# Performance work log

Measured on AMD Instinct MI355X. Metric: run time of the kernel, lower is better.

## Reference

```python
import jax, jax.numpy as jnp
import numpy as np
from jax import lax

N = 8192          # river-network nodes
B = 2             # batch
T = 1024          # time steps (hours)
W = 64            # max_delay (IRF support)
H = 256           # MLP hidden dim
DT = 1.0 / 24.0   # dt in days
D_LEVELS = 8      # tree depth (4-ary tree with 8192 nodes -> depths 0..7)
BRANCH = 4


def _tree():
    parent = np.zeros(N, np.int32)
    depth = np.zeros(N, np.int32)
    for i in range(1, N):
        p = (i - 1) // BRANCH
        parent[i] = p
        depth[i] = depth[p] + 1
    parent[0] = N  # root drains to dummy sink (row N is dropped after scatter)
    return parent, depth


def setup_inputs() -> dict:
    key = jax.random.key(0)
    ks = jax.random.split(key, 6)
    parent, depth = _tree()
    return {
        "x": jax.random.uniform(ks[0], (B, N, T), dtype=jnp.float32),
        "phys": jax.random.normal(ks[1], (N, 3), dtype=jnp.float32),
        "w1": jax.random.normal(ks[2], (3, H), dtype=jnp.float32) * 0.3,
        "b1": jnp.zeros((H,), jnp.float32),
        "w2": jax.random.normal(ks[3], (H, H), dtype=jnp.float32) * 0.05,
        "b2": jnp.zeros((H,), jnp.float32),
        "w3": jax.random.normal(ks[4], (H, 2), dtype=jnp.float32) * 0.05,
        "b3": jnp.zeros((2,), jnp.float32),
        "parent": jnp.asarray(parent),
        "depth": jnp.asarray(depth),
    }


def _mlp(phys, w1, b1, w2, b2, w3, b3):
    h = jax.nn.relu(phys @ w1 + b1)
    h = jax.nn.relu(h @ w2 + b2)
    return h @ w3 + b3  # [N, 2]


def _params(phys, w1, b1, w2, b2, w3, b3):
    raw = _mlp(phys, w1, b1, w2, b2, w3, b3)
    pre_sig_off = jnp.array([0.0, 3.0], jnp.float32)
    rng = jnp.array([0.25, 1.2], jnp.float32)
    off = jnp.array([0.005, 0.0], jnp.float32)
    p = jax.nn.sigmoid(raw - pre_sig_off) * rng + off
    return p[:, 0], p[:, 1]  # Muskingum k (days), x (weight)


def _muskingum_irf(k, xw):
    # Linear-channel Muskingum IRF: pure delay k*x then exponential store k*(1-x).
    t = jnp.arange(W, dtype=jnp.float32) * DT            # [W]
    delay = (k * xw)[:, None]                            # [N, 1]
    tau = jnp.maximum(k * (1.0 - xw), 0.5 * DT)[:, None]  # keep store positive
    h = jnp.where(t[None, :] >= delay,
                  jnp.exp(-(t[None, :] - delay) / tau) / tau, 0.0)
    return h / (h.sum(-1, keepdims=True) + 1e-8)          # [N, W], unit mass


def _causal_conv(sig, irf):
    # sig [B, N, T], irf [N, W]; depthwise causal conv along time per node.
    rhs = irf[:, None, ::-1]  # [N, 1, W], reversed so correlation == convolution
    return lax.conv_general_dilated(
        sig, rhs, window_strides=(1,), padding=[(W - 1, 0)],
        dimension_numbers=("NCH", "OIH", "NCH"), feature_group_count=N)


def _route(x, irf, parent, depth):
    # Leaves-to-root routing: out[i] = irf_i * (x[i] + sum_children out[child]).
    out = jnp.zeros_like(x)
    acc = x
    for d in range(D_LEVELS - 1, -1, -1):
        mask = (depth == d)[None, :, None]
        routed = _causal_conv(acc, irf)
        contrib = jnp.where(mask, routed, 0.0)
        out = out + contrib
        upd = jnp.zeros((B, N + 1, T), x.dtype).at[:, parent, :].add(contrib)
        acc = acc + upd[:, :N, :]
    return out


def reference(x, phys, w1, b1, w2, b2, w3, b3, parent, depth):
    k, xw = _params(phys, w1, b1, w2, b2, w3, b3)
    irf = _muskingum_irf(k, xw)
    return _route(x, irf, parent, depth)  # [B, N, T]
```

## Files before the change

### kernel.cpp

```cpp
#include <hip/hip_runtime.h>
#include <hip/hip_bf16.h>

#define NN 8192
#define TT 1024
#define WW 64
#define HH 256
#define DTF (1.0f/24.0f)

typedef __attribute__((ext_vector_type(8))) short short8_t;
typedef __attribute__((ext_vector_type(4))) short short4_t;
typedef __attribute__((ext_vector_type(4))) float f32x4_t;

__device__ __forceinline__ float sigmoidf_(float v) { return 1.0f / (1.0f + __expf(-v)); }

__device__ __forceinline__ short f2bf(float f) {
    __hip_bfloat16 h = __float2bfloat16(f);
    short s; __builtin_memcpy(&s, &h, sizeof(short));
    return s;
}

__device__ __forceinline__ int swz(int e) { return e ^ (((e >> 6) & 3) << 3); }

__global__ __launch_bounds__(256) void w2bf_kernel(
    const float* __restrict__ w2, short* __restrict__ w2f)
{
    const int gid  = blockIdx.x * 256 + threadIdx.x;
    const int ks   = gid >> 10;
    const int rest = gid & 1023;
    const int nt   = rest >> 6;
    const int lane = rest & 63;
    const int lg = lane >> 4, lc = lane & 15;
    short8_t v;
#pragma unroll
    for (int j = 0; j < 8; ++j)
        v[j] = f2bf(w2[(ks * 32 + 8 * lg + j) * HH + nt * 16 + lc]);
    *(short8_t*)&w2f[(size_t)gid * 8] = v;
}

__global__ __launch_bounds__(256) void mlp_mfma(
    const float* __restrict__ phys,
    const float* __restrict__ w1, const float* __restrict__ b1,
    const short* __restrict__ w2f, const float* __restrict__ b2,
    const float* __restrict__ w3, const float* __restrict__ b3,
    float* __restrict__ irf, short* __restrict__ irfB)
{
    const int t    = threadIdx.x;
    const int wv   = t >> 6;
    const int lane = t & 63;
    const int lc = lane & 15, lg = lane >> 4;
    const int n0 = blockIdx.x * 16;

    __shared__ float s_phys[16 * 3];
    __shared__ __align__(16) short s_h1b[16 * 256];
    __shared__ float s_red[4][16][2];
    __shared__ float s_kxw[16][2];
    __shared__ __align__(16) float s_irf[16 * 64];

    if (t < 48) s_phys[t] = phys[n0 * 3 + t];
    __syncthreads();

    {
        const int m  = t >> 4;
        const int i0 = (t & 15) * 16;
        const float p0 = s_phys[m*3+0], p1 = s_phys[m*3+1], p2 = s_phys[m*3+2];
        float h[16];
#pragma unroll
        for (int u = 0; u < 4; ++u) {
            const float4 a0 = *(const float4*)&w1[0*HH + i0 + 4*u];
            const float4 a1 = *(const float4*)&w1[1*HH + i0 + 4*u];
            const float4 a2 = *(const float4*)&w1[2*HH + i0 + 4*u];
            const float4 bb = *(const float4*)&b1[i0 + 4*u];
            h[4*u+0] = fmaxf(p0*a0.x + p1*a1.x + p2*a2.x + bb.x, 0.f);
            h[4*u+1] = fmaxf(p0*a0.y + p1*a1.y + p2*a2.y + bb.y, 0.f);
            h[4*u+2] = fmaxf(p0*a0.z + p1*a1.z + p2*a2.z + bb.z, 0.f);
            h[4*u+3] = fmaxf(p0*a0.w + p1*a1.w + p2*a2.w + bb.w, 0.f);
        }
#pragma unroll
        for (int u = 0; u < 2; ++u) {
            short8_t s;
#pragma unroll
            for (int j = 0; j < 8; ++j) s[j] = f2bf(h[8*u + j]);
            *(short8_t*)&s_h1b[m * 256 + ((i0 + 8*u) ^ ((m & 7) << 3))] = s;
        }
    }
    __syncthreads();

    f32x4_t acc[4];
#pragma unroll
    for (int u = 0; u < 4; ++u) acc[u] = f32x4_t{0.f, 0.f, 0.f, 0.f};
    short8_t af[8];
#pragma unroll
    for (int ks = 0; ks < 8; ++ks)
        af[ks] = *(const short8_t*)&s_h1b[lc * 256 + ((ks*32 + 8*lg) ^ ((lc & 7) << 3))];
#pragma unroll
    for (int u = 0; u < 4; ++u) {
        const int nt = 4 * wv + u;
#pragma unroll
        for (int ks = 0; ks < 8; ++ks) {
            const short8_t bfr = *(const short8_t*)&w2f[(size_t)((ks*16 + nt)*64 + lane) * 8];
            acc[u] = __builtin_amdgcn_mfma_f32_16x16x32_bf16(af[ks], bfr, acc[u], 0, 0, 0);
        }
    }

    float p3[4][2];
#pragma unroll
    for (int q = 0; q < 4; ++q) { p3[q][0] = 0.f; p3[q][1] = 0.f; }
#pragma unroll
    for (int u = 0; u < 4; ++u) {
        const int j = (4*wv + u) * 16 + lc;
        const float b2v = b2[j];
        const float w30 = w3[j*2+0], w31 = w3[j*2+1];
#pragma unroll
        for (int q = 0; q < 4; ++q) {
            const float h2 = fmaxf(acc[u][q] + b2v, 0.f);
            p3[q][0] += h2 * w30; p3[q][1] += h2 * w31;
        }
    }
#pragma unroll
    for (int off = 8; off >= 1; off >>= 1)
#pragma unroll
        for (int q = 0; q < 4; ++q) {
            p3[q][0] += __shfl_xor(p3[q][0], off);
            p3[q][1] += __shfl_xor(p3[q][1], off);
        }
    if (lc == 0)
#pragma unroll
        for (int q = 0; q < 4; ++q) {
            s_red[wv][4*lg + q][0] = p3[q][0];
            s_red[wv][4*lg + q][1] = p3[q][1];
        }
    __syncthreads();

    if (t < 32) {
        const int m = t >> 1, d = t & 1;
        const float raw = s_red[0][m][d] + s_red[1][m][d] + s_red[2][m][d] + s_red[3][m][d] + b3[d];
        s_kxw[m][d] = (d == 0) ? sigmoidf_(raw) * 0.25f + 0.005f
                               : sigmoidf_(raw - 3.f) * 1.2f;
    }
    __syncthreads();

    {
        const int nd = t >> 4, l = t & 15;
        const float k = s_kxw[nd][0], xw = s_kxw[nd][1];
        const float delay = k * xw;
        const float tau   = fmaxf(k * (1.f - xw), 0.5f * DTF);
        float hv[4]; float s = 0.f;
#pragma unroll
        for (int u = 0; u < 4; ++u) {
            const float tf = (l + 16*u) * DTF;
            hv[u] = (tf >= delay) ? __expf(-(tf - delay) / tau) / tau : 0.f;
            s += hv[u];
        }
#pragma unroll
        for (int off = 8; off >= 1; off >>= 1) s += __shfl_xor(s, off);
        const float inv = 1.f / (s + 1e-8f);
        float* drow = irf + (size_t)(n0 + nd) * WW;
#pragma unroll
        for (int u = 0; u < 4; ++u) {
            const float v = hv[u] * inv;
            drow[l + 16*u]        = v;
            s_irf[nd*64 + l + 16*u] = v;
        }
    }
    __syncthreads();

    {
        const int nd = t >> 4, lb = t & 15;
        const float* sr = &s_irf[nd * 64];
        short* dst = irfB + (size_t)(n0 + nd) * 1536;
#pragma unroll
        for (int li = 0; li < 4; ++li) {
            const int L = 4*lb + li;
            const int Llc = L & 15, Llg = L >> 4;
#pragma unroll
            for (int p = 0; p < 3; ++p) {
                short8_t v;
#pragma unroll
                for (int j = 0; j < 8; ++j) {
                    const int idx = Llc - 8*Llg - j + 16 + 32*p;
                    v[j] = f2bf((idx >= 0 && idx < 64) ? sr[idx & 63] : 0.f);
                }
                *(short8_t*)&dst[(size_t)(p*64 + L) * 8] = v;
            }
        }
    }
}

#define LROW 1152

__device__ __forceinline__ void zero_prologue(short* sab, int tid) {
    if (tid < 10) {
        short8_t z = {0,0,0,0,0,0,0,0};
        *(short8_t*)&sab[swz(8 * tid)] = z;
    }
}

__device__ __forceinline__ void load16(const float* __restrict__ src, int tid, float (&a)[16]) {
#pragma unroll
    for (int u = 0; u < 4; ++u) {
        const float4 v = *(const float4*)&src[16 * tid + 4 * u];
        a[4*u+0] = v.x; a[4*u+1] = v.y; a[4*u+2] = v.z; a[4*u+3] = v.w;
    }
}

__device__ __forceinline__ void stage16(short* sab, const float (&a)[16], int tid) {
#pragma unroll
    for (int u = 0; u < 2; ++u) {
        short8_t s;
#pragma unroll
        for (int j = 0; j < 8; ++j) s[j] = f2bf(a[8*u + j]);
        *(short8_t*)&sab[swz(80 + 16 * tid + 8 * u)] = s;
    }
}

__device__ __forceinline__ void load_bfrags(const short* __restrict__ irfB, int n,
                                            int tid, short8_t (&bf)[3]) {
#pragma unroll
    for (int p = 0; p < 3; ++p)
        bf[p] = *(const short8_t*)&irfB[(size_t)n * 1536 + (size_t)(p*64 + tid) * 8];
}

__device__ __forceinline__ void conv_mfma3(const short* sab, const short8_t (&bf)[3],
                                           int EB, f32x4_t (&acc)[4]) {
#pragma unroll
    for (int S = 0; S < 4; ++S) {
#pragma unroll
        for (int p = 0; p < 3; ++p) {
            const short8_t af = *(const short8_t*)&sab[swz(EB + 256 * S - 16 * (2 * p + 1))];
            acc[S] = __builtin_amdgcn_mfma_f32_16x16x32_bf16(bf[p], af, acc[S], 0, 0, 0);
        }
    }
}

__global__ __launch_bounds__(256) void route_lf6p(
    const float* __restrict__ x, const short* __restrict__ irfB,
    float* __restrict__ out)
{
    const int wid = threadIdx.x >> 6;
    const int tid = threadIdx.x & 63;
    const int r   = blockIdx.x * 4 + wid;
    if (r >= 3074) return;

    const int lc = tid & 15, lg = tid >> 4;
    const int EB = 80 + 16 * lc + 8 * lg;
    const int DP = 16 * lc + 4 * lg;

    __shared__ __align__(16) short s_a[4][LROW];
    short* sab = s_a[wid];
    zero_prologue(sab, tid);

    float a16[16];
    short8_t bf[3];

    if (r < 3072) {
        const bool isl6 = (r < 1366);
        const int idx = isl6 ? r : (r - 1366);
        const int b = idx & 1;
        const int n = __builtin_amdgcn_readfirstlane((isl6 ? 1365 : 512) + (idx >> 1));
        const size_t rowb = ((size_t)b * NN + n) * TT;
        const int c0 = 4 * n + 1;

        f32x4_t accD[4];
#pragma unroll
        for (int S = 0; S < 4; ++S)
            accD[S] = *(const f32x4_t*)&x[rowb + 256 * S + DP];

#pragma unroll 1
        for (int e = 0; e < 4; ++e) {
            const int c = c0 + e;
            if (c < NN) {
                const size_t crow = ((size_t)b * NN + c) * TT;
                load16(x + crow, tid, a16);
                stage16(sab, a16, tid);
                load_bfrags(irfB, c, tid, bf);
                f32x4_t accT[4];
#pragma unroll
                for (int S = 0; S < 4; ++S) accT[S] = f32x4_t{0.f, 0.f, 0.f, 0.f};
                conv_mfma3(sab, bf, EB, accT);
#pragma unroll
                for (int S = 0; S < 4; ++S) {
                    *(f32x4_t*)&out[crow + 256 * S + DP] = accT[S];
                    accD[S] += accT[S];
                }
            }
        }

#pragma unroll
        for (int S = 0; S < 4; ++S) {
            short4_t s4;
#pragma unroll
            for (int q = 0; q < 4; ++q) s4[q] = f2bf(accD[S][q]);
            *(short4_t*)&sab[swz(80 + 256 * S + DP)] = s4;
        }

        load_bfrags(irfB, n, tid, bf);
        f32x4_t accF[4];
#pragma unroll
        for (int S = 0; S < 4; ++S) accF[S] = f32x4_t{0.f, 0.f, 0.f, 0.f};
        conv_mfma3(sab, bf, EB, accF);
#pragma unroll
        for (int S = 0; S < 4; ++S)
            *(f32x4_t*)&out[rowb + 256 * S + DP] = accF[S];
    } else {
        const int idx = r - 3072;
        const int b = idx & 1;
        const int n = 2048;
        const size_t rowb = ((size_t)b * NN + n) * TT;

        load16(x + rowb, tid, a16);
        stage16(sab, a16, tid);
        load_bfrags(irfB, n, tid, bf);
        f32x4_t accF[4];
#pragma unroll
        for (int S = 0; S < 4; ++S) accF[S] = f32x4_t{0.f, 0.f, 0.f, 0.f};
        conv_mfma3(sab, bf, EB, accF);
#pragma unroll
        for (int S = 0; S < 4; ++S)
            *(f32x4_t*)&out[rowb + 256 * S + DP] = accF[S];
    }
}

__global__ __launch_bounds__(256) void route_mid_mfma(
    const float* __restrict__ x, const short* __restrict__ irfB,
    float* __restrict__ out, int base, int n_tasks)
{
    const int wid = threadIdx.x >> 6;
    const int tid = threadIdx.x & 63;
    const int r   = blockIdx.x * 4 + wid;
    if (r >= n_tasks) return;

    const int lc = tid & 15, lg = tid >> 4;
    const int EB = 80 + 16 * lc + 8 * lg;
    const int DP = 16 * lc + 4 * lg;

    __shared__ __align__(16) short s_a[4][LROW];
    short* sab = s_a[wid];
    zero_prologue(sab, tid);

    const int b = r & 1;
    const int n = __builtin_amdgcn_readfirstlane(base + (r >> 1));
    const size_t rowb = ((size_t)b * NN + n) * TT;
    const int c0 = 4 * n + 1;

    float a16[16];
#pragma unroll
    for (int u = 0; u < 4; ++u) {
        float4 v = *(const float4*)&x[rowb + 16 * tid + 4 * u];
#pragma unroll
        for (int e = 0; e < 4; ++e) {
            const float4 w = *(const float4*)&out[((size_t)b * NN + c0 + e) * TT + 16 * tid + 4 * u];
            v.x += w.x; v.y += w.y; v.z += w.z; v.w += w.w;
        }
        a16[4*u+0] = v.x; a16[4*u+1] = v.y; a16[4*u+2] = v.z; a16[4*u+3] = v.w;
    }
    stage16(sab, a16, tid);

    short8_t bf[3];
    load_bfrags(irfB, n, tid, bf);
    f32x4_t accF[4];
#pragma unroll
    for (int S = 0; S < 4; ++S) accF[S] = f32x4_t{0.f, 0.f, 0.f, 0.f};
    conv_mfma3(sab, bf, EB, accF);
#pragma unroll
    for (int S = 0; S < 4; ++S)
        *(f32x4_t*)&out[rowb + 256 * S + DP] = accF[S];
}

__global__ __launch_bounds__(256) void route_tail3_mfma(
    const float* __restrict__ x, const short* __restrict__ irfB,
    float* __restrict__ out)
{
    const int wid = threadIdx.x >> 6;
    const int tid = threadIdx.x & 63;
    const int b   = blockIdx.x & 1;
    const int p   = 5 + (int)(blockIdx.x >> 1);

    const int lc = tid & 15, lg = tid >> 4;
    const int EB = 80 + 16 * lc + 8 * lg;
    const int DP = 16 * lc + 4 * lg;

    __shared__ __align__(16) short s_a[4][LROW];
    __shared__ __align__(16) float s_ch[4][TT];
    short* sab = s_a[wid];
    zero_prologue(sab, tid);

    const int cw = 4 * p + 1 + wid;
    const size_t crow = ((size_t)b * NN + cw) * TT;

    float a16[16];
    short8_t bf[3];

    f32x4_t accCW[4];
#pragma unroll
    for (int S = 0; S < 4; ++S)
        accCW[S] = *(const f32x4_t*)&x[crow + 256 * S + DP];

#pragma unroll 1
    for (int k = 0; k < 4; ++k) {
        const int g = 4 * cw + 1 + k;
        const size_t grow = ((size_t)b * NN + g) * TT;
#pragma unroll
        for (int u = 0; u < 4; ++u) {
            float4 v = *(const float4*)&x[grow + 16 * tid + 4 * u];
#pragma unroll
            for (int e = 0; e < 4; ++e) {
                const float4 w = *(const float4*)&out[((size_t)b * NN + (4 * g + 1 + e)) * TT + 16 * tid + 4 * u];
                v.x += w.x; v.y += w.y; v.z += w.z; v.w += w.w;
            }
            a16[4*u+0] = v.x; a16[4*u+1] = v.y; a16[4*u+2] = v.z; a16[4*u+3] = v.w;
        }
        stage16(sab, a16, tid);
        load_bfrags(irfB, g, tid, bf);
        f32x4_t accT[4];
#pragma unroll
        for (int S = 0; S < 4; ++S) accT[S] = f32x4_t{0.f, 0.f, 0.f, 0.f};
        conv_mfma3(sab, bf, EB, accT);
#pragma unroll
        for (int S = 0; S < 4; ++S) {
            *(f32x4_t*)&out[grow + 256 * S + DP] = accT[S];
            accCW[S] += accT[S];
        }
    }

#pragma unroll
    for (int S = 0; S < 4; ++S) {
        short4_t s4;
#pragma unroll
        for (int q = 0; q < 4; ++q) s4[q] = f2bf(accCW[S][q]);
        *(short4_t*)&sab[swz(80 + 256 * S + DP)] = s4;
    }
    load_bfrags(irfB, cw, tid, bf);
    f32x4_t accB[4];
#pragma unroll
    for (int S = 0; S < 4; ++S) accB[S] = f32x4_t{0.f, 0.f, 0.f, 0.f};
    conv_mfma3(sab, bf, EB, accB);
#pragma unroll
    for (int S = 0; S < 4; ++S) {
        *(f32x4_t*)&out[crow + 256 * S + DP] = accB[S];
        *(f32x4_t*)&s_ch[wid][256 * S + DP]  = accB[S];
    }

    __syncthreads();

    if (wid == 0) {
        const size_t prow = ((size_t)b * NN + p) * TT;
#pragma unroll
        for (int u = 0; u < 4; ++u) {
            float4 v = *(const float4*)&x[prow + 16 * tid + 4 * u];
#pragma unroll
            for (int w2 = 0; w2 < 4; ++w2) {
                const float4 cc = *(const float4*)&s_ch[w2][16 * tid + 4 * u];
                v.x += cc.x; v.y += cc.y; v.z += cc.z; v.w += cc.w;
            }
            a16[4*u+0] = v.x; a16[4*u+1] = v.y; a16[4*u+2] = v.z; a16[4*u+3] = v.w;
        }
        stage16(sab, a16, tid);
        load_bfrags(irfB, p, tid, bf);
        f32x4_t accF[4];
#pragma unroll
        for (int S = 0; S < 4; ++S) accF[S] = f32x4_t{0.f, 0.f, 0.f, 0.f};
        conv_mfma3(sab, bf, EB, accF);
#pragma unroll
        for (int S = 0; S < 4; ++S)
            *(f32x4_t*)&out[prow + 256 * S + DP] = accF[S];
    }
}

__device__ __forceinline__ void load_rf(const float* __restrict__ irf, int n, float (&rf)[WW]) {
    const float* irp = irf + (size_t)n * WW;
#pragma unroll
    for (int i = 0; i < WW / 4; ++i) {
        const float4 f = *(const float4*)&irp[4 * i];
        rf[4*i+0] = f.x; rf[4*i+1] = f.y; rf[4*i+2] = f.z; rf[4*i+3] = f.w;
    }
}

__device__ __forceinline__ void wave_conv16(const float (&a)[16], const float (&rf)[WW],
                                            float (&y)[16], int tid)
{
#pragma unroll
    for (int j = 0; j < 16; ++j) y[j] = 0.0f;
#pragma unroll
    for (int m = 0; m < 16; ++m)
#pragma unroll
        for (int j = m; j < 16; ++j)
            y[j] += rf[j - m] * a[m];
#pragma unroll
    for (int d = 1; d <= 4; ++d) {
        float h[16];
#pragma unroll
        for (int m = 0; m < 16; ++m) {
            const float ha = __shfl(a[m], tid - d);
            h[m] = (tid >= d) ? ha : 0.0f;
        }
        if (d < 4) {
#pragma unroll
            for (int m = 0; m < 16; ++m)
#pragma unroll
                for (int j = 0; j < 16; ++j)
                    y[j] += rf[j + 16 * d - m] * h[m];
        } else {
#pragma unroll
            for (int m = 1; m < 16; ++m)
#pragma unroll
                for (int j = 0; j < m; ++j)
                    y[j] += rf[j + WW - m] * h[m];
        }
    }
}

__global__ __launch_bounds__(256) void route_tail2(
    const float* __restrict__ x, const float* __restrict__ irf,
    float* __restrict__ out)
{
    const int wid = threadIdx.x >> 6;
    const int tid = threadIdx.x & 63;
    const int b   = blockIdx.x;

    __shared__ __align__(16) float s_ch[4][TT];

    const int cw = 1 + wid;
    const size_t crow = ((size_t)b * NN + cw) * TT;
    const int loc = tid * 16;

    float rf[WW], a[16], y[16];

#pragma unroll
    for (int u = 0; u < 4; ++u) {
        float4 v = *(const float4*)&x[crow + loc + 4 * u];
#pragma unroll
        for (int e = 0; e < 4; ++e) {
            const float4 w = *(const float4*)&out[((size_t)b * NN + (4 * cw + 1 + e)) * TT + loc + 4 * u];
            v.x += w.x; v.y += w.y; v.z += w.z; v.w += w.w;
        }
        a[4*u+0] = v.x; a[4*u+1] = v.y; a[4*u+2] = v.z; a[4*u+3] = v.w;
    }
    load_rf(irf, cw, rf);
    wave_conv16(a, rf, y, tid);
#pragma unroll
    for (int u = 0; u < 4; ++u) {
        const float4 f = make_float4(y[4*u+0], y[4*u+1], y[4*u+2], y[4*u+3]);
        *(float4*)&out[crow + loc + 4 * u] = f;
        *(float4*)&s_ch[wid][loc + 4 * u]  = f;
    }

    __syncthreads();

    if (wid == 0) {
        const size_t prow = (size_t)b * NN * TT;
#pragma unroll
        for (int u = 0; u < 4; ++u) {
            float4 v = *(const float4*)&x[prow + loc + 4 * u];
#pragma unroll
            for (int w2 = 0; w2 < 4; ++w2) {
                const float4 cc = *(const float4*)&s_ch[w2][loc + 4 * u];
                v.x += cc.x; v.y += cc.y; v.z += cc.z; v.w += cc.w;
            }
            a[4*u+0] = v.x; a[4*u+1] = v.y; a[4*u+2] = v.z; a[4*u+3] = v.w;
        }
        load_rf(irf, 0, rf);
        wave_conv16(a, rf, y, tid);
#pragma unroll
        for (int u = 0; u < 4; ++u)
            *(float4*)&out[prow + loc + 4 * u] = make_float4(y[4*u+0], y[4*u+1], y[4*u+2], y[4*u+3]);
    }
}

extern "C" void kernel_launch(void* const* d_in, const int* in_sizes, int n_in,
                              void* d_out, int out_size, void* d_ws, size_t ws_size,
                              hipStream_t stream) {
    const float* x    = (const float*)d_in[0];
    const float* phys = (const float*)d_in[1];
    const float* w1   = (const float*)d_in[2];
    const float* b1   = (const float*)d_in[3];
    const float* w2   = (const float*)d_in[4];
    const float* b2   = (const float*)d_in[5];
    const float* w3   = (const float*)d_in[6];
    const float* b3   = (const float*)d_in[7];

    float* out = (float*)d_out;
    float* irf  = (float*)d_ws;
    short* w2f  = (short*)((char*)d_ws + (2u << 20));
    short* irfB = (short*)((char*)d_ws + (4u << 20));

    w2bf_kernel<<<32, 256, 0, stream>>>(w2, w2f);
    mlp_mfma<<<512, 256, 0, stream>>>(phys, w1, b1, w2f, b2, w3, b3, irf, irfB);

    route_lf6p<<<(3074 + 3) / 4, 256, 0, stream>>>(x, irfB, out);
    route_mid_mfma<<<(342 + 3) / 4, 256, 0, stream>>>(x, irfB, out, 341, 342);
    route_tail3_mfma<<<32, 256, 0, stream>>>(x, irfB, out);
    route_tail2<<<2, 256, 0, stream>>>(x, irf, out);
}
```

Baseline: 79.49 us.

## Split each leaf-parent routing task across two wavefronts with LDS reduction

Each level-6/level-5 parent task is now handled by a pair of wavefronts, each convolving two of the four children, with partial sums combined through shared memory before the parent's own convolution. The grid doubles to 1537 blocks of two tasks each, and the special n=2048 case is folded into the common path. This shortens the serial per-wave chain of child convolutions and raises the number of active waves, at the cost of a block-wide barrier, extra LDS, and one of the two waves sitting idle during the final convolution.

After: 80.73 us. About the same (+1.6%).

```diff
diff --git a/kernel.cpp b/kernel.cpp
--- a/kernel.cpp
+++ b/kernel.cpp
@@ -232,83 +232,88 @@
     }
 }
 
-__global__ __launch_bounds__(256) void route_lf6p(
+__global__ __launch_bounds__(256) void route_lf6p2(
     const float* __restrict__ x, const short* __restrict__ irfB,
     float* __restrict__ out)
 {
-    const int wid = threadIdx.x >> 6;
-    const int tid = threadIdx.x & 63;
-    const int r   = blockIdx.x * 4 + wid;
-    if (r >= 3074) return;
+    const int wid   = threadIdx.x >> 6;
+    const int tid   = threadIdx.x & 63;
+    const int pairI = wid >> 1;
+    const int w     = wid & 1;
+    const int r     = blockIdx.x * 2 + pairI;
 
     const int lc = tid & 15, lg = tid >> 4;
     const int EB = 80 + 16 * lc + 8 * lg;
     const int DP = 16 * lc + 4 * lg;
 
     __shared__ __align__(16) short s_a[4][LROW];
+    __shared__ __align__(16) float s_pacc[2][TT];
     short* sab = s_a[wid];
     zero_prologue(sab, tid);
 
-    float a16[16];
-    short8_t bf[3];
-
+    int n, b;
     if (r < 3072) {
         const bool isl6 = (r < 1366);
         const int idx = isl6 ? r : (r - 1366);
-        const int b = idx & 1;
-        const int n = __builtin_amdgcn_readfirstlane((isl6 ? 1365 : 512) + (idx >> 1));
-        const size_t rowb = ((size_t)b * NN + n) * TT;
-        const int c0 = 4 * n + 1;
-
-        f32x4_t accD[4];
+        b = idx & 1;
+        n = (isl6 ? 1365 : 512) + (idx >> 1);
+    } else {
+        b = r - 3072;
+        n = 2048;
+    }
+    n = __builtin_amdgcn_readfirstlane(n);
+    const size_t rowb = ((size_t)b * NN + n) * TT;
+    const int c0 = 4 * n + 1;
+
+    float a16[16];
+    short8_t bf[3];
+
+    f32x4_t accD[4];
+    if (w == 0) {
 #pragma unroll
         for (int S = 0; S < 4; ++S)
             accD[S] = *(const f32x4_t*)&x[rowb + 256 * S + DP];
+    } else {
+#pragma unroll
+        for (int S = 0; S < 4; ++S) accD[S] = f32x4_t{0.f, 0.f, 0.f, 0.f};
+    }
 
 #pragma unroll 1
-        for (int e = 0; e < 4; ++e) {
-            const int c = c0 + e;
-            if (c < NN) {
-                const size_t crow = ((size_t)b * NN + c) * TT;
-                load16(x + crow, tid, a16);
-                stage16(sab, a16, tid);
-                load_bfrags(irfB, c, tid, bf);
-                f32x4_t accT[4];
-#pragma unroll
-                for (int S = 0; S < 4; ++S) accT[S] = f32x4_t{0.f, 0.f, 0.f, 0.f};
-                conv_mfma3(sab, bf, EB, accT);
-#pragma unroll
-                for (int S = 0; S < 4; ++S) {
-                    *(f32x4_t*)&out[crow + 256 * S + DP] = accT[S];
-                    accD[S] += accT[S];
-                }
+    for (int ee = 0; ee < 2; ++ee) {
+        const int c = c0 + 2 * w + ee;
+        if (c < NN) {
+            const size_t crow = ((size_t)b * NN + c) * TT;
+            load16(x + crow, tid, a16);
+            stage16(sab, a16, tid);
+            load_bfrags(irfB, c, tid, bf);
+            f32x4_t accT[4];
+#pragma unroll
+            for (int S = 0; S < 4; ++S) accT[S] = f32x4_t{0.f, 0.f, 0.f, 0.f};
+            conv_mfma3(sab, bf, EB, accT);
+#pragma unroll
+            for (int S = 0; S < 4; ++S) {
+                *(f32x4_t*)&out[crow + 256 * S + DP] = accT[S];
+                accD[S] += accT[S];
             }
         }
-
+    }
+
+    if (w == 1) {
+#pragma unroll
+        for (int S = 0; S < 4; ++S)
+            *(f32x4_t*)&s_pacc[pairI][256 * S + DP] = accD[S];
+    }
+    __syncthreads();
+
+    if (w == 0) {
 #pragma unroll
         for (int S = 0; S < 4; ++S) {
+            const f32x4_t pp = *(const f32x4_t*)&s_pacc[pairI][256 * S + DP];
             short4_t s4;
 #pragma unroll
-            for (int q = 0; q < 4; ++q) s4[q] = f2bf(accD[S][q]);
+            for (int q = 0; q < 4; ++q) s4[q] = f2bf(accD[S][q] + pp[q]);
             *(short4_t*)&sab[swz(80 + 256 * S + DP)] = s4;
         }
-
-        load_bfrags(irfB, n, tid, bf);
-        f32x4_t accF[4];
-#pragma unroll
-        for (int S = 0; S < 4; ++S) accF[S] = f32x4_t{0.f, 0.f, 0.f, 0.f};
-        conv_mfma3(sab, bf, EB, accF);
-#pragma unroll
-        for (int S = 0; S < 4; ++S)
-            *(f32x4_t*)&out[rowb + 256 * S + DP] = accF[S];
-    } else {
-        const int idx = r - 3072;
-        const int b = idx & 1;
-        const int n = 2048;
-        const size_t rowb = ((size_t)b * NN + n) * TT;
-
-        load16(x + rowb, tid, a16);
-        stage16(sab, a16, tid);
         load_bfrags(irfB, n, tid, bf);
         f32x4_t accF[4];
 #pragma unroll
@@ -586,7 +591,7 @@
     w2bf_kernel<<<32, 256, 0, stream>>>(w2, w2f);
     mlp_mfma<<<512, 256, 0, stream>>>(phys, w1, b1, w2f, b2, w3, b3, irf, irfB);
 
-    route_lf6p<<<(3074 + 3) / 4, 256, 0, stream>>>(x, irfB, out);
+    route_lf6p2<<<1537, 256, 0, stream>>>(x, irfB, out);
     route_mid_mfma<<<(342 + 3) / 4, 256, 0, stream>>>(x, irfB, out, 341, 342);
     route_tail3_mfma<<<32, 256, 0, stream>>>(x, irfB, out);
     route_tail2<<<2, 256, 0, stream>>>(x, irf, out);
```
